# Kernel tuning notes

Hardware: AMD Instinct MI355X
Metric: run time of the kernel (lower is better)

## Reference

```python
import jax, jax.numpy as jnp
import numpy as np
from jax import lax

L, T, DM, DH = 4, 4096, 2048, 1024
MAX_PHASE = 6.28
EPS = 1e-5


def setup_inputs() -> dict:
    key = jax.random.key(0)
    ks = jax.random.split(key, 16)
    # LRU initializers (r_min=0, r_max=1)
    u1 = jax.random.uniform(ks[0], (L, DH))
    nu_log = jnp.log(-0.5 * jnp.log(u1))
    u2 = jax.random.uniform(ks[1], (L, DH))
    theta_log = jnp.log(MAX_PHASE * u2)
    abs_lam = jnp.exp(-jnp.exp(nu_log))  # |lambda|
    gamma_log = jnp.log(jnp.sqrt(1.0 - abs_lam ** 2))
    B_re = jax.random.normal(ks[2], (L, DH, DM)) / np.sqrt(2 * DM)
    B_im = jax.random.normal(ks[3], (L, DH, DM)) / np.sqrt(2 * DM)
    C_re = jax.random.normal(ks[4], (L, DM, DH)) / np.sqrt(DH)
    C_im = jax.random.normal(ks[5], (L, DM, DH)) / np.sqrt(DH)
    D = jax.random.normal(ks[6], (L, DM))
    bound = 1.0 / np.sqrt(DM)
    enc_w = jax.random.uniform(ks[7], (DM, DM), minval=-bound, maxval=bound)
    enc_b = jax.random.uniform(ks[8], (DM,), minval=-bound, maxval=bound)
    out1_w = jax.random.uniform(ks[9], (L, DM, DM), minval=-bound, maxval=bound)
    out1_b = jax.random.uniform(ks[10], (L, DM), minval=-bound, maxval=bound)
    out2_w = jax.random.uniform(ks[11], (L, DM, DM), minval=-bound, maxval=bound)
    out2_b = jax.random.uniform(ks[12], (L, DM), minval=-bound, maxval=bound)
    norm_w = jnp.ones((L, DM))
    norm_b = jnp.zeros((L, DM))
    x = jax.random.normal(ks[13], (T, DM))
    return dict(x=x, enc_w=enc_w, enc_b=enc_b, nu_log=nu_log, theta_log=theta_log,
                gamma_log=gamma_log, B_re=B_re, B_im=B_im, C_re=C_re, C_im=C_im,
                D=D, norm_w=norm_w, norm_b=norm_b, out1_w=out1_w, out1_b=out1_b,
                out2_w=out2_w, out2_b=out2_b)


def _lru(xn, nu, th, gl, br, bi, cr, ci, d):
    # xn: (T, DM) real -> (T, DM) real
    lam = jnp.exp(-jnp.exp(nu) + 1j * jnp.exp(th))          # (DH,) complex
    B_norm = (br + 1j * bi) * jnp.exp(gl)[:, None]           # (DH, DM)
    Bu = xn.astype(B_norm.dtype) @ B_norm.T                  # (T, DH) complex
    a = jnp.broadcast_to(lam, Bu.shape)
    def combine(e1, e2):
        a1, b1 = e1
        a2, b2 = e2
        return a1 * a2, a2 * b1 + b2
    _, h = lax.associative_scan(combine, (a, Bu), axis=0)    # h_t = lam*h_{t-1} + Bu_t
    C = cr + 1j * ci
    return (h @ C.T).real + xn * d


def _batchnorm(x, w, b):
    # training-mode BatchNorm1d over dim 0 (biased variance), matching torch
    mu = x.mean(axis=0)
    var = jnp.mean((x - mu) ** 2, axis=0)
    return (x - mu) / jnp.sqrt(var + EPS) * w + b


def _forward(x, enc_w, enc_b, nu_log, theta_log, gamma_log, B_re, B_im,
             C_re, C_im, D, norm_w, norm_b, out1_w, out1_b, out2_w, out2_b):
    x = x @ enc_w.T + enc_b
    def layer(carry, p):
        nu, th, gl, br, bi, cr, ci, d, nw, nb, w1, b1, w2, b2 = p
        xn = _batchnorm(carry, nw, nb)
        y = _lru(xn, nu, th, gl, br, bi, cr, ci, d)
        y = jax.nn.gelu(y, approximate=False)
        y = (y @ w1.T + b1) * jax.nn.sigmoid(y @ w2.T + b2)
        return carry + y, None
    x, _ = lax.scan(layer, x, (nu_log, theta_log, gamma_log, B_re, B_im,
                               C_re, C_im, D, norm_w, norm_b,
                               out1_w, out1_b, out2_w, out2_b))
    return x


def reference(x, enc_w, enc_b, nu_log, theta_log, gamma_log, B_re, B_im,
              C_re, C_im, D, norm_w, norm_b, out1_w, out1_b, out2_w, out2_b):
    return _forward(x, enc_w, enc_b, nu_log, theta_log, gamma_log, B_re, B_im,
                    C_re, C_im, D, norm_w, norm_b, out1_w, out1_b, out2_w, out2_b)
```

## Files before the change

### kernel.cpp

```cpp
#include <hip/hip_runtime.h>
#include <stdint.h>
#include <math.h>


#define LAYERS 4
#define TT     4096
#define DMODEL 2048
#define DHID   1024
#define NCHUNK 64
#define CLEN   64
#define KTILES 64

typedef unsigned short ushort_t;
typedef __attribute__((ext_vector_type(8))) _Float16 half8;
typedef __attribute__((ext_vector_type(4))) float    f32x4;

__device__ __forceinline__ unsigned pack2h(float a, float b) {
  _Float16 ha = (_Float16)a, hb = (_Float16)b;
  unsigned short ua = *(unsigned short*)&ha, ub = *(unsigned short*)&hb;
  return (unsigned)ua | ((unsigned)ub << 16);
}

__global__ __launch_bounds__(256)
void convert_h(const float* __restrict__ B0, const float* __restrict__ B1,
               int ldb, int NS, int KS, ushort_t* __restrict__ Hi)
{
  __shared__ float tile[128][33];
  const int mb  = blockIdx.x;
  const int kb  = blockIdx.y;
  const int tid = threadIdx.x;
  const int r0  = tid >> 3;
  const int c0  = (tid & 7) * 4;
#pragma unroll
  for (int rep = 0; rep < 4; ++rep) {
    const int rr = rep * 32 + r0;
    const int n  = mb * 128 + rr;
    const int k  = kb * 32 + c0;
    const float* bp; long idx;
    if (n >= NS)      { bp = B1; idx = (long)(n - NS) * ldb + k; }
    else if (k >= KS) { bp = B1; idx = (long)n * ldb + (k - KS); }
    else              { bp = B0; idx = (long)n * ldb + k; }
#pragma unroll
    for (int u = 0; u < 4; ++u) tile[rr][c0 + u] = bp[idx + u];
  }
  __syncthreads();
#pragma unroll
  for (int rep = 0; rep < 2; ++rep) {
    const int id2 = rep * 256 + tid;
    const int kg  = id2 >> 7;
    const int m   = id2 & 127;
    const long off = ((long)mb * KTILES + kb) * 4096 + (kg * 128 + m) * 8;
    unsigned hw[4];
#pragma unroll
    for (int p = 0; p < 4; ++p)
      hw[p] = pack2h(tile[m][kg * 8 + p * 2], tile[m][kg * 8 + p * 2 + 1]);
    *(uint4*)&Hi[off] = make_uint4(hw[0], hw[1], hw[2], hw[3]);
  }
}

__global__ __launch_bounds__(256)
void bn_convert(const float* __restrict__ carry, const float* __restrict__ stats,
                const float* __restrict__ nw, const float* __restrict__ nb,
                ushort_t* __restrict__ Hi)
{
  __shared__ float tile[128][33];
  const int mb  = blockIdx.x;
  const int kb  = blockIdx.y;
  const int tid = threadIdx.x;
  const int r0  = tid >> 3;
  const int c0  = (tid & 7) * 4;
  float mean[4], rstd[4], w_[4], b_[4];
#pragma unroll
  for (int u = 0; u < 4; ++u) {
    const int j = kb * 32 + c0 + u;
    const float mu = stats[j] * (1.0f / TT);
    const float va = fmaxf(stats[DMODEL + j] * (1.0f / TT) - mu * mu, 0.0f);
    mean[u] = mu; rstd[u] = rsqrtf(va + 1e-5f);
    w_[u] = nw[j]; b_[u] = nb[j];
  }
#pragma unroll
  for (int rep = 0; rep < 4; ++rep) {
    const int rr  = rep * 32 + r0;
    const long base = (long)(mb * 128 + rr) * 2048 + kb * 32 + c0;
#pragma unroll
    for (int u = 0; u < 4; ++u)
      tile[rr][c0 + u] = (carry[base + u] - mean[u]) * rstd[u] * w_[u] + b_[u];
  }
  __syncthreads();
#pragma unroll
  for (int rep = 0; rep < 2; ++rep) {
    const int id2 = rep * 256 + tid;
    const int kg  = id2 >> 7;
    const int m   = id2 & 127;
    const long off = ((long)mb * KTILES + kb) * 4096 + (kg * 128 + m) * 8;
    unsigned hw[4];
#pragma unroll
    for (int p = 0; p < 4; ++p)
      hw[p] = pack2h(tile[m][kg * 8 + p * 2], tile[m][kg * 8 + p * 2 + 1]);
    *(uint4*)&Hi[off] = make_uint4(hw[0], hw[1], hw[2], hw[3]);
  }
}

__global__ __launch_bounds__(256)
void scan3_convert(const float* __restrict__ loc,
                   const float* __restrict__ ccre, const float* __restrict__ ccim,
                   const float* __restrict__ nu_log, const float* __restrict__ th_log,
                   ushort_t* __restrict__ Hi)
{
  __shared__ float tile[128][33];
  const int mb  = blockIdx.x;
  const int kb  = blockIdx.y;
  const int tid = threadIdx.x;
  const int r0  = tid >> 3;
  const int c0  = (tid & 7) * 4;
  const int isim = (kb >= 32);
  const int c0l  = (mb * 2) & 1023;
  (void)c0l;
  float en[4], eth[4], cr0[4], ci0[4], cr1[4], ci1[4];
#pragma unroll
  for (int u = 0; u < 4; ++u) {
    const int col = kb * 32 + c0 + u;
    const int h   = col & 1023;
    en[u]  = expf(nu_log[h]);
    eth[u] = expf(th_log[h]);
    const int ch0 = mb * 2, ch1 = mb * 2 + 1;
    cr0[u] = ccre[ch0 * DHID + h]; ci0[u] = ccim[ch0 * DHID + h];
    cr1[u] = ccre[ch1 * DHID + h]; ci1[u] = ccim[ch1 * DHID + h];
  }
#pragma unroll
  for (int rep = 0; rep < 4; ++rep) {
    const int rr  = rep * 32 + r0;
    const int sel = rr >> 6;
    const float p = (float)((rr & 63) + 1);
    const long base = (long)(mb * 128 + rr) * 2048 + kb * 32 + c0;
#pragma unroll
    for (int u = 0; u < 4; ++u) {
      const float magp = expf(-p * en[u]);
      const float ang  = p * eth[u];
      float sv, cv;
      __sincosf(ang, &sv, &cv);
      const float pr = magp * cv, pi = magp * sv;
      const float cr_ = sel ? cr1[u] : cr0[u];
      const float ci_ = sel ? ci1[u] : ci0[u];
      const float L = loc[base + u];
      const float v = isim ? -(L + pr * ci_ + pi * cr_)
                           :  (L + pr * cr_ - pi * ci_);
      tile[rr][c0 + u] = v;
    }
  }
  __syncthreads();
#pragma unroll
  for (int rep = 0; rep < 2; ++rep) {
    const int id2 = rep * 256 + tid;
    const int kg  = id2 >> 7;
    const int m   = id2 & 127;
    const long off = ((long)mb * KTILES + kb) * 4096 + (kg * 128 + m) * 8;
    unsigned hw[4];
#pragma unroll
    for (int p2 = 0; p2 < 4; ++p2)
      hw[p2] = pack2h(tile[m][kg * 8 + p2 * 2], tile[m][kg * 8 + p2 * 2 + 1]);
    *(uint4*)&Hi[off] = make_uint4(hw[0], hw[1], hw[2], hw[3]);
  }
}

__global__ __launch_bounds__(256)
void e1_convert(const float* __restrict__ y, const ushort_t* __restrict__ xnT,
                const float* __restrict__ d, ushort_t* __restrict__ Hi)
{
  __shared__ float tile[128][33];
  const int mb  = blockIdx.x;
  const int kb  = blockIdx.y;
  const int tid = threadIdx.x;
  const int r0  = tid >> 3;
  const int c0  = (tid & 7) * 4;
#pragma unroll
  for (int rep = 0; rep < 4; ++rep) {
    const int rr  = rep * 32 + r0;
    const long base = (long)(mb * 128 + rr) * 2048 + kb * 32 + c0;
#pragma unroll
    for (int u = 0; u < 4; ++u) tile[rr][c0 + u] = y[base + u];
  }
  __syncthreads();
#pragma unroll
  for (int rep = 0; rep < 2; ++rep) {
    const int id2 = rep * 256 + tid;
    const int kg  = id2 >> 7;
    const int m   = id2 & 127;
    const long off = ((long)mb * KTILES + kb) * 4096 + (kg * 128 + m) * 8;
    const half8 xh = *(const half8*)&xnT[off];
    const float* dp = d + kb * 32 + kg * 8;
    unsigned hw[4];
#pragma unroll
    for (int p = 0; p < 4; ++p) {
      float g2[2];
#pragma unroll
      for (int e = 0; e < 2; ++e) {
        const int j = p * 2 + e;
        const float v = tile[m][kg * 8 + j] + (float)xh[j] * dp[j];
        g2[e] = 0.5f * v * (1.0f + erff(v * 0.70710678118654752440f));
      }
      hw[p] = pack2h(g2[0], g2[1]);
    }
    *(uint4*)&Hi[off] = make_uint4(hw[0], hw[1], hw[2], hw[3]);
  }
}

#define GLDS(gp, lp) __builtin_amdgcn_global_load_lds( \
    (__attribute__((address_space(1))) void*)(void*)(gp), \
    (__attribute__((address_space(3))) void*)(lp), 16, 0, 0)

__global__ __launch_bounds__(256)
void gemm_mfma(const ushort_t* __restrict__ Ahi, const ushort_t* __restrict__ Bhi,
               float* __restrict__ C, const float* __restrict__ bias,
               int epi, float* __restrict__ stats)
{
  __shared__ ushort_t S[2][16384];
  const int tid  = threadIdx.x;
  const int lane = tid & 63;
  const int wid  = tid >> 6;
  const int wm   = wid >> 1;
  const int wn   = wid & 1;

  const int bid = blockIdx.y * gridDim.x + blockIdx.x;
  const int xcd = bid & 7, idx = bid >> 3;
  const int mb  = ((xcd & 3) << 3) | (idx & 7);
  const int nb  = ((xcd >> 2) << 3) | (idx >> 3);

  f32x4 acc[4][4];
#pragma unroll
  for (int i = 0; i < 4; ++i)
#pragma unroll
    for (int j = 0; j < 4; ++j) acc[i][j] = (f32x4){0.f, 0.f, 0.f, 0.f};

  const ushort_t* ga = Ahi + (long)mb * KTILES * 4096 + tid * 8;
  const ushort_t* gb = Bhi + (long)nb * KTILES * 4096 + tid * 8;

  const int albase = ((lane >> 4) * 128 + wm * 64 + (lane & 15)) * 8;
  const int blbase = ((lane >> 4) * 128 + wn * 64 + (lane & 15)) * 8;

  half8 A0[4], B0[4], A1[4], B1[4];

#define STAGE(P) \
  GLDS(ga,        &S[P][tid * 8]); \
  GLDS(ga + 2048, &S[P][2048 + tid * 8]); \
  GLDS(ga + 4096, &S[P][4096 + tid * 8]); \
  GLDS(ga + 6144, &S[P][6144 + tid * 8]); \
  GLDS(gb,        &S[P][8192 + tid * 8]); \
  GLDS(gb + 2048, &S[P][10240 + tid * 8]); \
  GLDS(gb + 4096, &S[P][12288 + tid * 8]); \
  GLDS(gb + 6144, &S[P][14336 + tid * 8]); \
  ga += 8192; gb += 8192;

#define RD(P) \
  _Pragma("unroll") \
  for (int m = 0; m < 4; ++m) A0[m] = *(const half8*)&S[P][albase + m * 128]; \
  _Pragma("unroll") \
  for (int n = 0; n < 4; ++n) B0[n] = *(const half8*)&S[P][8192 + blbase + n * 128]; \
  _Pragma("unroll") \
  for (int m = 0; m < 4; ++m) A1[m] = *(const half8*)&S[P][4096 + albase + m * 128]; \
  _Pragma("unroll") \
  for (int n = 0; n < 4; ++n) B1[n] = *(const half8*)&S[P][12288 + blbase + n * 128];

#define MFMA16(A_, B_) \
  _Pragma("unroll") \
  for (int m = 0; m < 4; ++m) \
    _Pragma("unroll") \
    for (int n = 0; n < 4; ++n) \
      acc[m][n] = __builtin_amdgcn_mfma_f32_16x16x32_f16(A_[m], B_[n], acc[m][n], 0, 0, 0);

#define WAIT_VM_BAR(n) asm volatile("s_waitcnt vmcnt(" #n ")" ::: "memory"); \
  __builtin_amdgcn_sched_barrier(0); __builtin_amdgcn_s_barrier();
#define LGKM0_BAR asm volatile("s_waitcnt lgkmcnt(0)" ::: "memory"); \
  __builtin_amdgcn_sched_barrier(0); __builtin_amdgcn_s_barrier();

#define KSTEP(P) \
  WAIT_VM_BAR(8) \
  RD(P) \
  __builtin_amdgcn_s_setprio(1); \
  MFMA16(A0, B0) \
  MFMA16(A1, B1) \
  __builtin_amdgcn_s_setprio(0); \
  LGKM0_BAR \
  STAGE(P)

  STAGE(0)
  STAGE(1)
  for (int it = 0; it < 15; ++it) {
    KSTEP(0)
    KSTEP(1)
  }
  WAIT_VM_BAR(8)
  RD(0)
  __builtin_amdgcn_s_setprio(1);
  MFMA16(A0, B0)
  MFMA16(A1, B1)
  __builtin_amdgcn_s_setprio(0);
  WAIT_VM_BAR(0)
  RD(1)
  __builtin_amdgcn_s_setprio(1);
  MFMA16(A0, B0)
  MFMA16(A1, B1)
  __builtin_amdgcn_s_setprio(0);
#undef STAGE
#undef RD
#undef MFMA16
#undef WAIT_VM_BAR
#undef LGKM0_BAR
#undef KSTEP

  const int cn = lane & 15;
  const int cr = (lane >> 4) * 4;
  float s0[4] = {0.f, 0.f, 0.f, 0.f}, s1[4] = {0.f, 0.f, 0.f, 0.f};
#pragma unroll
  for (int m = 0; m < 4; ++m) {
    const long row = (long)mb * 128 + wm * 64 + m * 16 + cr;
#pragma unroll
    for (int n = 0; n < 4; ++n) {
      const int col = nb * 128 + wn * 64 + n * 16 + cn;
      const float bv = bias ? bias[col] : 0.0f;
      if (epi == 0) {
#pragma unroll
        for (int q = 0; q < 4; ++q) {
          const float v = acc[m][n][q] + bv;
          C[(row + q) * 2048 + col] = v;
          s0[n] += v; s1[n] += v * v;
        }
      } else {
#pragma unroll
        for (int q = 0; q < 4; ++q)
          C[(row + q) * 2048 + col] = acc[m][n][q] + bv;
      }
    }
  }
  if (stats) {
    __syncthreads();
    float* sred = (float*)&S[0][0];
    if (tid < 256) sred[tid] = 0.f;
    __syncthreads();
#pragma unroll
    for (int n = 0; n < 4; ++n) {
      const int lc = wn * 64 + n * 16 + cn;
      atomicAdd(&sred[lc], s0[n]);
      atomicAdd(&sred[128 + lc], s1[n]);
    }
    __syncthreads();
    if (tid < 128) {
      atomicAdd(&stats[nb * 128 + tid], sred[tid]);
      atomicAdd(&stats[DMODEL + nb * 128 + tid], sred[128 + tid]);
    }
  }
}

__global__ __launch_bounds__(256)
void gemm_dual(const ushort_t* __restrict__ Ahi, const ushort_t* __restrict__ B1t,
               const ushort_t* __restrict__ B2t,
               float* __restrict__ carry, const float* __restrict__ b1,
               const float* __restrict__ b2, float* __restrict__ stats)
{
  __shared__ ushort_t S[3][8192];
  const int tid  = threadIdx.x;
  const int lane = tid & 63;
  const int wid  = tid >> 6;
  const int wm   = wid >> 1;
  const int wn   = wid & 1;

  const int bid = blockIdx.y * gridDim.x + blockIdx.x;
  const int xcd = bid & 7, idx = bid >> 3;
  const int mb  = ((xcd & 3) << 3) | (idx & 7);
  const int nbb = ((xcd >> 2) << 4) | (idx >> 3);

  f32x4 acc1[4][2], acc2[4][2];
#pragma unroll
  for (int i = 0; i < 4; ++i)
#pragma unroll
    for (int j = 0; j < 2; ++j) {
      acc1[i][j] = (f32x4){0.f, 0.f, 0.f, 0.f};
      acc2[i][j] = (f32x4){0.f, 0.f, 0.f, 0.f};
    }

  const int nt = nbb >> 1;
  const int hb = nbb & 1;

  const ushort_t* ga = Ahi + (long)mb * KTILES * 4096 + tid * 8;
  const long boff = ((tid >> 6) * 128 + hb * 64 + (tid & 63)) * 8;
  const ushort_t* g1 = B1t + (long)nt * KTILES * 4096 + boff;
  const ushort_t* g2 = B2t + (long)nt * KTILES * 4096 + boff;

  const int albase = ((lane >> 4) * 128 + wm * 64 + (lane & 15)) * 8;
  const int blbase = ((lane >> 4) * 64 + wn * 32 + (lane & 15)) * 8;

  half8 Af[4], B1f[2], B2f[2];

#define STAGE(P) \
  GLDS(ga,        &S[P][tid * 8]); \
  GLDS(ga + 2048, &S[P][2048 + tid * 8]); \
  GLDS(g1,        &S[P][4096 + tid * 8]); \
  GLDS(g2,        &S[P][6144 + tid * 8]); \
  ga += 4096; g1 += 4096; g2 += 4096;

#define RD(P) \
  _Pragma("unroll") \
  for (int m = 0; m < 4; ++m) Af[m]  = *(const half8*)&S[P][albase + m * 128]; \
  _Pragma("unroll") \
  for (int n = 0; n < 2; ++n) B1f[n] = *(const half8*)&S[P][4096 + blbase + n * 128]; \
  _Pragma("unroll") \
  for (int n = 0; n < 2; ++n) B2f[n] = *(const half8*)&S[P][6144 + blbase + n * 128];

#define MFMA16D \
  __builtin_amdgcn_s_setprio(1); \
  _Pragma("unroll") \
  for (int m = 0; m < 4; ++m) \
    _Pragma("unroll") \
    for (int n = 0; n < 2; ++n) \
      acc1[m][n] = __builtin_amdgcn_mfma_f32_16x16x32_f16(Af[m], B1f[n], acc1[m][n], 0, 0, 0); \
  _Pragma("unroll") \
  for (int m = 0; m < 4; ++m) \
    _Pragma("unroll") \
    for (int n = 0; n < 2; ++n) \
      acc2[m][n] = __builtin_amdgcn_mfma_f32_16x16x32_f16(Af[m], B2f[n], acc2[m][n], 0, 0, 0); \
  __builtin_amdgcn_s_setprio(0);

#define WAITB(n) asm volatile("s_waitcnt vmcnt(" #n ") lgkmcnt(0)" ::: "memory"); \
  __builtin_amdgcn_sched_barrier(0); __builtin_amdgcn_s_barrier();

#define KSTEPD(PRD, PST) \
  WAITB(4) \
  STAGE(PST) \
  RD(PRD) \
  MFMA16D

  STAGE(0)
  STAGE(1)
  for (int it = 0; it < 20; ++it) {
    KSTEPD(0, 2)
    KSTEPD(1, 0)
    KSTEPD(2, 1)
  }
  KSTEPD(0, 2)
  KSTEPD(1, 0)
  WAITB(4)
  RD(2)
  MFMA16D
  WAITB(0)
  RD(0)
  MFMA16D
#undef STAGE
#undef RD
#undef MFMA16D
#undef WAITB
#undef KSTEPD

  const int cn = lane & 15;
  const int cr = (lane >> 4) * 4;
  float s0[2] = {0.f, 0.f}, s1[2] = {0.f, 0.f};
#pragma unroll
  for (int m = 0; m < 4; ++m) {
    const long row = (long)mb * 128 + wm * 64 + m * 16 + cr;
#pragma unroll
    for (int n = 0; n < 2; ++n) {
      const int col = nbb * 64 + wn * 32 + n * 16 + cn;
      const float b1v = b1[col], b2v = b2[col];
#pragma unroll
      for (int q = 0; q < 4; ++q) {
        const long idx2 = (row + q) * 2048 + col;
        const float t1v = acc1[m][n][q] + b1v;
        const float t2v = acc2[m][n][q] + b2v;
        const float v = carry[idx2] + t1v * (1.0f / (1.0f + expf(-t2v)));
        carry[idx2] = v;
        s0[n] += v; s1[n] += v * v;
      }
    }
  }
  if (stats) {
    __syncthreads();
    float* sred = (float*)&S[0][0];
    if (tid < 128) sred[tid] = 0.f;
    __syncthreads();
#pragma unroll
    for (int n = 0; n < 2; ++n) {
      const int lc = wn * 32 + n * 16 + cn;
      atomicAdd(&sred[lc], s0[n]);
      atomicAdd(&sred[64 + lc], s1[n]);
    }
    __syncthreads();
    if (tid < 64) {
      atomicAdd(&stats[nbb * 64 + tid], sred[tid]);
      atomicAdd(&stats[DMODEL + nbb * 64 + tid], sred[64 + tid]);
    }
  }
}

__device__ __forceinline__ void get_lam(const float* nu_log, const float* th_log,
                                        int h, float& lre, float& lim)
{
  const float mag = expf(-expf(nu_log[h]));
  const float th  = expf(th_log[h]);
  lre = mag * cosf(th);
  lim = mag * sinf(th);
}

__global__ void scan1(float* __restrict__ bu,
                      const float* __restrict__ nu_log, const float* __restrict__ th_log,
                      const float* __restrict__ gl_log)
{
  const int gid = blockIdx.x * 256 + threadIdx.x;
  const int c = gid >> 10, h = gid & 1023;
  float lre, lim; get_lam(nu_log, th_log, h, lre, lim);
  const float gamma = expf(gl_log[h]);
  float hr = 0.f, hi = 0.f;
  for (int i = 0; i < CLEN; ++i) {
    const long t = (long)c * CLEN + i;
    const float br_ = bu[t * 2048 + h] * gamma;
    const float bi_ = bu[t * 2048 + 1024 + h] * gamma;
    const float nr = lre * hr - lim * hi + br_;
    const float ni = lre * hi + lim * hr + bi_;
    hr = nr; hi = ni;
    bu[t * 2048 + h] = hr;
    bu[t * 2048 + 1024 + h] = hi;
  }
}

__global__ void scan2(const float* __restrict__ loc,
                      float* __restrict__ ccre, float* __restrict__ ccim,
                      const float* __restrict__ nu_log, const float* __restrict__ th_log)
{
  const int h = blockIdx.x * 256 + threadIdx.x;
  float lre, lim; get_lam(nu_log, th_log, h, lre, lim);
  float ar = lre, ai = lim;
  for (int s = 0; s < 6; ++s) { float nr = ar * ar - ai * ai, ni = 2.f * ar * ai; ar = nr; ai = ni; }
  float er = 0.f, ei = 0.f;
  for (int c = 0; c < NCHUNK; ++c) {
    ccre[c * DHID + h] = er; ccim[c * DHID + h] = ei;
    const long t = (long)c * CLEN + (CLEN - 1);
    const float nr = ar * er - ai * ei + loc[t * 2048 + h];
    const float ni = ar * ei + ai * er + loc[t * 2048 + 1024 + h];
    er = nr; ei = ni;
  }
}

__global__ void finalize(const float* __restrict__ carry, float* __restrict__ out)
{
  const long idx = (long)blockIdx.x * 256 + threadIdx.x;
  const float v = carry[idx];
  out[idx] = (v == v && fabsf(v) < 3.0e38f) ? v : 300000.0f;
}

__global__ void diagfill(float* __restrict__ out, float val)
{
  const long idx = (long)blockIdx.x * 256 + threadIdx.x;
  out[idx] = (idx == 0) ? val : 0.0f;
}

extern "C" void kernel_launch(void* const* d_in, const int* in_sizes, int n_in,
                              void* d_out, int out_size, void* d_ws, size_t ws_size,
                              hipStream_t stream)
{
  (void)out_size;
  const int EW = (TT * DMODEL) / 256;
  float* out = (float*)d_out;

  if (n_in != 17 || in_sizes[0] != TT * DMODEL) {
    diagfill<<<EW, 256, 0, stream>>>(out, (float)(1 << 18));
    return;
  }
  if (ws_size < 151600000ull) {
    diagfill<<<EW, 256, 0, stream>>>(out, (float)(1 << 12));
    return;
  }

  const float* x     = (const float*)d_in[0];
  const float* enc_w = (const float*)d_in[1];
  const float* enc_b = (const float*)d_in[2];
  const float* nu    = (const float*)d_in[3];
  const float* th    = (const float*)d_in[4];
  const float* gl    = (const float*)d_in[5];
  const float* Bre   = (const float*)d_in[6];
  const float* Bim   = (const float*)d_in[7];
  const float* Cre   = (const float*)d_in[8];
  const float* Cim   = (const float*)d_in[9];
  const float* Dd    = (const float*)d_in[10];
  const float* nw    = (const float*)d_in[11];
  const float* nb    = (const float*)d_in[12];
  const float* w1    = (const float*)d_in[13];
  const float* b1    = (const float*)d_in[14];
  const float* w2    = (const float*)d_in[15];
  const float* b2    = (const float*)d_in[16];

  char* ws = (char*)d_ws;
  float*    carry = (float*)(ws);
  ushort_t* AhiX  = (ushort_t*)(ws + 33554432);
  float*    buf1  = (float*)(ws + 67108864);
  ushort_t* Ahi   = (ushort_t*)(ws + 100663296);
  ushort_t* B2hi  = (ushort_t*)(ws + 117440512);
  ushort_t* Bhi   = (ushort_t*)(ws + 134217728);
  float*    ccre  = (float*)(ws + 150994944);
  float*    ccim  = (float*)(ws + 151257088);
  float*    stats = (float*)(ws + 151519232);

  const dim3 gcA(32, 64);
  const dim3 gcW(16, 64);
  const dim3 gg(32, 16);
  const dim3 gg2(32, 32);
  const int BIG = 1 << 30;

  hipMemsetAsync(stats, 0, 2 * DMODEL * sizeof(float), stream);
  convert_h<<<gcA, 256, 0, stream>>>(x, x, 2048, BIG, BIG, Ahi);
  convert_h<<<gcW, 256, 0, stream>>>(enc_w, enc_w, 2048, BIG, BIG, Bhi);
  gemm_mfma<<<gg, 256, 0, stream>>>(Ahi, Bhi, carry, enc_b, 0, stats);

  for (int l = 0; l < LAYERS; ++l) {
    const float* Brl = Bre + (size_t)l * DHID * DMODEL;
    const float* Bil = Bim + (size_t)l * DHID * DMODEL;
    const float* Crl = Cre + (size_t)l * DMODEL * DHID;
    const float* Cil = Cim + (size_t)l * DMODEL * DHID;
    const float* w1l = w1 + (size_t)l * DMODEL * DMODEL;
    const float* w2l = w2 + (size_t)l * DMODEL * DMODEL;

    bn_convert<<<gcA, 256, 0, stream>>>(carry, stats, nw + l * DMODEL,
                                        nb + l * DMODEL, AhiX);

    convert_h<<<gcW, 256, 0, stream>>>(Brl, Bil, 2048, 1024, BIG, Bhi);
    gemm_mfma<<<gg, 256, 0, stream>>>(AhiX, Bhi, buf1, nullptr, 3, nullptr);

    scan1<<<256, 256, 0, stream>>>(buf1, nu + l * DHID, th + l * DHID, gl + l * DHID);
    scan2<<<4, 256, 0, stream>>>(buf1, ccre, ccim, nu + l * DHID, th + l * DHID);

    convert_h<<<gcW, 256, 0, stream>>>(Crl, Cil, 1024, BIG, 1024, Bhi);
    scan3_convert<<<gcA, 256, 0, stream>>>(buf1, ccre, ccim, nu + l * DHID,
                                           th + l * DHID, Ahi);

    gemm_mfma<<<gg, 256, 0, stream>>>(Ahi, Bhi, buf1, nullptr, 3, nullptr);

    e1_convert<<<gcA, 256, 0, stream>>>(buf1, AhiX, Dd + l * DMODEL, Ahi);

    convert_h<<<gcW, 256, 0, stream>>>(w1l, w1l, 2048, BIG, BIG, Bhi);
    convert_h<<<gcW, 256, 0, stream>>>(w2l, w2l, 2048, BIG, BIG, B2hi);
    float* nstats = (l < LAYERS - 1) ? stats : nullptr;
    if (nstats) hipMemsetAsync(stats, 0, 2 * DMODEL * sizeof(float), stream);
    gemm_dual<<<gg2, 256, 0, stream>>>(Ahi, Bhi, B2hi, carry,
                                       b1 + l * DMODEL, b2 + l * DMODEL, nstats);
  }

  finalize<<<EW, 256, 0, stream>>>(carry, out);
}
```

Baseline: 1.307 ms.

## Fuse chunk-local LRU scan and GELU convert into GEMM epilogues with interleaved re/im layout

```diff
diff --git a/kernel.cpp b/kernel.cpp
--- a/kernel.cpp
+++ b/kernel.cpp
@@ -19,6 +19,15 @@
   _Float16 ha = (_Float16)a, hb = (_Float16)b;
   unsigned short ua = *(unsigned short*)&ha, ub = *(unsigned short*)&hb;
   return (unsigned)ua | ((unsigned)ub << 16);
+}
+
+__device__ __forceinline__ void get_lam(const float* nu_log, const float* th_log,
+                                        int h, float& lre, float& lim)
+{
+  const float mag = expf(-expf(nu_log[h]));
+  const float th  = expf(th_log[h]);
+  lre = mag * cosf(th);
+  lim = mag * sinf(th);
 }
 
 __global__ __launch_bounds__(256)
@@ -59,6 +68,75 @@
 }
 
 __global__ __launch_bounds__(256)
+void convert_ilv_rows(const float* __restrict__ P0, const float* __restrict__ P1,
+                      int ldb, ushort_t* __restrict__ Hi)
+{
+  __shared__ float tile[128][33];
+  const int mb  = blockIdx.x;
+  const int kb  = blockIdx.y;
+  const int tid = threadIdx.x;
+  const int r0  = tid >> 3;
+  const int c0  = (tid & 7) * 4;
+#pragma unroll
+  for (int rep = 0; rep < 4; ++rep) {
+    const int rr = rep * 32 + r0;
+    const int n  = mb * 128 + rr;
+    const float* bp = (n & 1) ? P1 : P0;
+    const long idx = (long)(n >> 1) * ldb + kb * 32 + c0;
+#pragma unroll
+    for (int u = 0; u < 4; ++u) tile[rr][c0 + u] = bp[idx + u];
+  }
+  __syncthreads();
+#pragma unroll
+  for (int rep = 0; rep < 2; ++rep) {
+    const int id2 = rep * 256 + tid;
+    const int kg  = id2 >> 7;
+    const int m   = id2 & 127;
+    const long off = ((long)mb * KTILES + kb) * 4096 + (kg * 128 + m) * 8;
+    unsigned hw[4];
+#pragma unroll
+    for (int p = 0; p < 4; ++p)
+      hw[p] = pack2h(tile[m][kg * 8 + p * 2], tile[m][kg * 8 + p * 2 + 1]);
+    *(uint4*)&Hi[off] = make_uint4(hw[0], hw[1], hw[2], hw[3]);
+  }
+}
+
+__global__ __launch_bounds__(256)
+void convert_ilv_cols(const float* __restrict__ P0, const float* __restrict__ P1,
+                      int ldb, ushort_t* __restrict__ Hi)
+{
+  __shared__ float tile[128][33];
+  const int mb  = blockIdx.x;
+  const int kb  = blockIdx.y;
+  const int tid = threadIdx.x;
+  const int r0  = tid >> 3;
+  const int c0  = (tid & 7) * 4;
+#pragma unroll
+  for (int rep = 0; rep < 4; ++rep) {
+    const int rr = rep * 32 + r0;
+    const int n  = mb * 128 + rr;
+    const long base = (long)n * ldb + ((kb * 32 + c0) >> 1);
+    tile[rr][c0 + 0] = P0[base];
+    tile[rr][c0 + 1] = P1[base];
+    tile[rr][c0 + 2] = P0[base + 1];
+    tile[rr][c0 + 3] = P1[base + 1];
+  }
+  __syncthreads();
+#pragma unroll
+  for (int rep = 0; rep < 2; ++rep) {
+    const int id2 = rep * 256 + tid;
+    const int kg  = id2 >> 7;
+    const int m   = id2 & 127;
+    const long off = ((long)mb * KTILES + kb) * 4096 + (kg * 128 + m) * 8;
+    unsigned hw[4];
+#pragma unroll
+    for (int p = 0; p < 4; ++p)
+      hw[p] = pack2h(tile[m][kg * 8 + p * 2], tile[m][kg * 8 + p * 2 + 1]);
+    *(uint4*)&Hi[off] = make_uint4(hw[0], hw[1], hw[2], hw[3]);
+  }
+}
+
+__global__ __launch_bounds__(256)
 void bn_convert(const float* __restrict__ carry, const float* __restrict__ stats,
                 const float* __restrict__ nw, const float* __restrict__ nb,
                 ushort_t* __restrict__ Hi)
@@ -113,19 +191,17 @@
   const int tid = threadIdx.x;
   const int r0  = tid >> 3;
   const int c0  = (tid & 7) * 4;
-  const int isim = (kb >= 32);
-  const int c0l  = (mb * 2) & 1023;
-  (void)c0l;
   float en[4], eth[4], cr0[4], ci0[4], cr1[4], ci1[4];
+  int   im[4];
 #pragma unroll
   for (int u = 0; u < 4; ++u) {
     const int col = kb * 32 + c0 + u;
-    const int h   = col & 1023;
+    const int h   = col >> 1;
+    im[u]  = col & 1;
     en[u]  = expf(nu_log[h]);
     eth[u] = expf(th_log[h]);
-    const int ch0 = mb * 2, ch1 = mb * 2 + 1;
-    cr0[u] = ccre[ch0 * DHID + h]; ci0[u] = ccim[ch0 * DHID + h];
-    cr1[u] = ccre[ch1 * DHID + h]; ci1[u] = ccim[ch1 * DHID + h];
+    cr0[u] = ccre[(mb * 2) * DHID + h];     ci0[u] = ccim[(mb * 2) * DHID + h];
+    cr1[u] = ccre[(mb * 2 + 1) * DHID + h]; ci1[u] = ccim[(mb * 2 + 1) * DHID + h];
   }
 #pragma unroll
   for (int rep = 0; rep < 4; ++rep) {
@@ -143,9 +219,8 @@
       const float cr_ = sel ? cr1[u] : cr0[u];
       const float ci_ = sel ? ci1[u] : ci0[u];
       const float L = loc[base + u];
-      const float v = isim ? -(L + pr * ci_ + pi * cr_)
-                           :  (L + pr * cr_ - pi * ci_);
-      tile[rr][c0 + u] = v;
+      tile[rr][c0 + u] = im[u] ? -(L + pr * ci_ + pi * cr_)
+                               :  (L + pr * cr_ - pi * ci_);
     }
   }
   __syncthreads();
@@ -163,48 +238,6 @@
   }
 }
 
-__global__ __launch_bounds__(256)
-void e1_convert(const float* __restrict__ y, const ushort_t* __restrict__ xnT,
-                const float* __restrict__ d, ushort_t* __restrict__ Hi)
-{
-  __shared__ float tile[128][33];
-  const int mb  = blockIdx.x;
-  const int kb  = blockIdx.y;
-  const int tid = threadIdx.x;
-  const int r0  = tid >> 3;
-  const int c0  = (tid & 7) * 4;
-#pragma unroll
-  for (int rep = 0; rep < 4; ++rep) {
-    const int rr  = rep * 32 + r0;
-    const long base = (long)(mb * 128 + rr) * 2048 + kb * 32 + c0;
-#pragma unroll
-    for (int u = 0; u < 4; ++u) tile[rr][c0 + u] = y[base + u];
-  }
-  __syncthreads();
-#pragma unroll
-  for (int rep = 0; rep < 2; ++rep) {
-    const int id2 = rep * 256 + tid;
-    const int kg  = id2 >> 7;
-    const int m   = id2 & 127;
-    const long off = ((long)mb * KTILES + kb) * 4096 + (kg * 128 + m) * 8;
-    const half8 xh = *(const half8*)&xnT[off];
-    const float* dp = d + kb * 32 + kg * 8;
-    unsigned hw[4];
-#pragma unroll
-    for (int p = 0; p < 4; ++p) {
-      float g2[2];
-#pragma unroll
-      for (int e = 0; e < 2; ++e) {
-        const int j = p * 2 + e;
-        const float v = tile[m][kg * 8 + j] + (float)xh[j] * dp[j];
-        g2[e] = 0.5f * v * (1.0f + erff(v * 0.70710678118654752440f));
-      }
-      hw[p] = pack2h(g2[0], g2[1]);
-    }
-    *(uint4*)&Hi[off] = make_uint4(hw[0], hw[1], hw[2], hw[3]);
-  }
-}
-
 #define GLDS(gp, lp) __builtin_amdgcn_global_load_lds( \
     (__attribute__((address_space(1))) void*)(void*)(gp), \
     (__attribute__((address_space(3))) void*)(lp), 16, 0, 0)
@@ -212,7 +245,11 @@
 __global__ __launch_bounds__(256)
 void gemm_mfma(const ushort_t* __restrict__ Ahi, const ushort_t* __restrict__ Bhi,
                float* __restrict__ C, const float* __restrict__ bias,
-               int epi, float* __restrict__ stats)
+               int epi, float* __restrict__ stats,
+               ushort_t* __restrict__ gT,
+               const float* __restrict__ dvec,
+               const float* __restrict__ nu_log, const float* __restrict__ th_log,
+               const float* __restrict__ gl_log)
 {
   __shared__ ushort_t S[2][16384];
   const int tid  = threadIdx.x;
@@ -310,43 +347,105 @@
 
   const int cn = lane & 15;
   const int cr = (lane >> 4) * 4;
-  float s0[4] = {0.f, 0.f, 0.f, 0.f}, s1[4] = {0.f, 0.f, 0.f, 0.f};
-#pragma unroll
-  for (int m = 0; m < 4; ++m) {
-    const long row = (long)mb * 128 + wm * 64 + m * 16 + cr;
-#pragma unroll
-    for (int n = 0; n < 4; ++n) {
-      const int col = nb * 128 + wn * 64 + n * 16 + cn;
-      const float bv = bias ? bias[col] : 0.0f;
-      if (epi == 0) {
+
+  if (epi == 0) {
+    float s0[4] = {0.f, 0.f, 0.f, 0.f}, s1[4] = {0.f, 0.f, 0.f, 0.f};
+#pragma unroll
+    for (int m = 0; m < 4; ++m) {
+      const long row = (long)mb * 128 + wm * 64 + m * 16 + cr;
+#pragma unroll
+      for (int n = 0; n < 4; ++n) {
+        const int col = nb * 128 + wn * 64 + n * 16 + cn;
+        const float bv = bias ? bias[col] : 0.0f;
 #pragma unroll
         for (int q = 0; q < 4; ++q) {
           const float v = acc[m][n][q] + bv;
           C[(row + q) * 2048 + col] = v;
           s0[n] += v; s1[n] += v * v;
         }
-      } else {
-#pragma unroll
-        for (int q = 0; q < 4; ++q)
-          C[(row + q) * 2048 + col] = acc[m][n][q] + bv;
       }
     }
-  }
-  if (stats) {
-    __syncthreads();
-    float* sred = (float*)&S[0][0];
-    if (tid < 256) sred[tid] = 0.f;
-    __syncthreads();
+    if (stats) {
+      __syncthreads();
+      float* sred = (float*)&S[0][0];
+      if (tid < 256) sred[tid] = 0.f;
+      __syncthreads();
+#pragma unroll
+      for (int n = 0; n < 4; ++n) {
+        const int lc = wn * 64 + n * 16 + cn;
+        atomicAdd(&sred[lc], s0[n]);
+        atomicAdd(&sred[128 + lc], s1[n]);
+      }
+      __syncthreads();
+      if (tid < 128) {
+        atomicAdd(&stats[nb * 128 + tid], sred[tid]);
+        atomicAdd(&stats[DMODEL + nb * 128 + tid], sred[128 + tid]);
+      }
+    }
+    return;
+  }
+
+  __syncthreads();
+  float* Lf = (float*)&S[0][0];
+#pragma unroll
+  for (int m = 0; m < 4; ++m) {
+    const int r = wm * 64 + m * 16 + cr;
 #pragma unroll
     for (int n = 0; n < 4; ++n) {
-      const int lc = wn * 64 + n * 16 + cn;
-      atomicAdd(&sred[lc], s0[n]);
-      atomicAdd(&sred[128 + lc], s1[n]);
-    }
-    __syncthreads();
+      const int c = wn * 64 + n * 16 + cn;
+#pragma unroll
+      for (int q = 0; q < 4; ++q)
+        Lf[(r + q) * 128 + c] = acc[m][n][q];
+    }
+  }
+  __syncthreads();
+
+  if (epi == 1) {
     if (tid < 128) {
-      atomicAdd(&stats[nb * 128 + tid], sred[tid]);
-      atomicAdd(&stats[DMODEL + nb * 128 + tid], sred[128 + tid]);
+      const int p  = tid & 63;
+      const int ch = tid >> 6;
+      const int hg = nb * 64 + p;
+      const float gamma = expf(gl_log[hg]);
+      float lre, lim; get_lam(nu_log, th_log, hg, lre, lim);
+      float hr = 0.f, hi = 0.f;
+      const long base = ((long)mb * 128 + ch * 64) * 2048 + nb * 128 + 2 * p;
+      for (int i = 0; i < 64; ++i) {
+        const float br_ = Lf[(ch * 64 + i) * 128 + 2 * p]     * gamma;
+        const float bi_ = Lf[(ch * 64 + i) * 128 + 2 * p + 1] * gamma;
+        const float nr = lre * hr - lim * hi + br_;
+        const float ni = lre * hi + lim * hr + bi_;
+        hr = nr; hi = ni;
+        *(float2*)&C[base + (long)i * 2048] = make_float2(hr, hi);
+      }
+    }
+    return;
+  }
+
+  {
+    const int cb = nb * 4;
+#pragma unroll
+    for (int c = 0; c < 8; ++c) {
+      const int chunk = c * 256 + tid;
+      const int m  = chunk & 127;
+      const int kg = (chunk >> 7) & 3;
+      const int lt = chunk >> 9;
+      const long off = ((long)mb * KTILES + cb + lt) * 4096 + (kg * 128 + m) * 8;
+      const half8 xh = *(const half8*)&gT[off];
+      const float* Lrow = &Lf[m * 128 + lt * 32 + kg * 8];
+      const float* dp = dvec + nb * 128 + lt * 32 + kg * 8;
+      unsigned hw[4];
+#pragma unroll
+      for (int p = 0; p < 4; ++p) {
+        float g2[2];
+#pragma unroll
+        for (int e = 0; e < 2; ++e) {
+          const int j = p * 2 + e;
+          const float v = Lrow[j] + (float)xh[j] * dp[j];
+          g2[e] = 0.5f * v * (1.0f + erff(v * 0.70710678118654752440f));
+        }
+        hw[p] = pack2h(g2[0], g2[1]);
+      }
+      *(uint4*)&gT[off] = make_uint4(hw[0], hw[1], hw[2], hw[3]);
     }
   }
 }
@@ -490,36 +589,6 @@
   }
 }
 
-__device__ __forceinline__ void get_lam(const float* nu_log, const float* th_log,
-                                        int h, float& lre, float& lim)
-{
-  const float mag = expf(-expf(nu_log[h]));
-  const float th  = expf(th_log[h]);
-  lre = mag * cosf(th);
-  lim = mag * sinf(th);
-}
-
-__global__ void scan1(float* __restrict__ bu,
-                      const float* __restrict__ nu_log, const float* __restrict__ th_log,
-                      const float* __restrict__ gl_log)
-{
-  const int gid = blockIdx.x * 256 + threadIdx.x;
-  const int c = gid >> 10, h = gid & 1023;
-  float lre, lim; get_lam(nu_log, th_log, h, lre, lim);
-  const float gamma = expf(gl_log[h]);
-  float hr = 0.f, hi = 0.f;
-  for (int i = 0; i < CLEN; ++i) {
-    const long t = (long)c * CLEN + i;
-    const float br_ = bu[t * 2048 + h] * gamma;
-    const float bi_ = bu[t * 2048 + 1024 + h] * gamma;
-    const float nr = lre * hr - lim * hi + br_;
-    const float ni = lre * hi + lim * hr + bi_;
-    hr = nr; hi = ni;
-    bu[t * 2048 + h] = hr;
-    bu[t * 2048 + 1024 + h] = hi;
-  }
-}
-
 __global__ void scan2(const float* __restrict__ loc,
                       float* __restrict__ ccre, float* __restrict__ ccim,
                       const float* __restrict__ nu_log, const float* __restrict__ th_log)
@@ -532,8 +601,8 @@
   for (int c = 0; c < NCHUNK; ++c) {
     ccre[c * DHID + h] = er; ccim[c * DHID + h] = ei;
     const long t = (long)c * CLEN + (CLEN - 1);
-    const float nr = ar * er - ai * ei + loc[t * 2048 + h];
-    const float ni = ar * ei + ai * er + loc[t * 2048 + 1024 + h];
+    const float nr = ar * er - ai * ei + loc[t * 2048 + 2 * h];
+    const float ni = ar * ei + ai * er + loc[t * 2048 + 2 * h + 1];
     er = nr; ei = ni;
   }
 }
@@ -606,7 +675,8 @@
   hipMemsetAsync(stats, 0, 2 * DMODEL * sizeof(float), stream);
   convert_h<<<gcA, 256, 0, stream>>>(x, x, 2048, BIG, BIG, Ahi);
   convert_h<<<gcW, 256, 0, stream>>>(enc_w, enc_w, 2048, BIG, BIG, Bhi);
-  gemm_mfma<<<gg, 256, 0, stream>>>(Ahi, Bhi, carry, enc_b, 0, stats);
+  gemm_mfma<<<gg, 256, 0, stream>>>(Ahi, Bhi, carry, enc_b, 0, stats,
+                                    nullptr, nullptr, nullptr, nullptr, nullptr);
 
   for (int l = 0; l < LAYERS; ++l) {
     const float* Brl = Bre + (size_t)l * DHID * DMODEL;
@@ -619,25 +689,26 @@
     bn_convert<<<gcA, 256, 0, stream>>>(carry, stats, nw + l * DMODEL,
                                         nb + l * DMODEL, AhiX);
 
-    convert_h<<<gcW, 256, 0, stream>>>(Brl, Bil, 2048, 1024, BIG, Bhi);
-    gemm_mfma<<<gg, 256, 0, stream>>>(AhiX, Bhi, buf1, nullptr, 3, nullptr);
-
-    scan1<<<256, 256, 0, stream>>>(buf1, nu + l * DHID, th + l * DHID, gl + l * DHID);
+    convert_ilv_rows<<<gcW, 256, 0, stream>>>(Brl, Bil, 2048, Bhi);
+    gemm_mfma<<<gg, 256, 0, stream>>>(AhiX, Bhi, buf1, nullptr, 1, nullptr,
+                                      nullptr, nullptr,
+                                      nu + l * DHID, th + l * DHID, gl + l * DHID);
+
     scan2<<<4, 256, 0, stream>>>(buf1, ccre, ccim, nu + l * DHID, th + l * DHID);
 
-    convert_h<<<gcW, 256, 0, stream>>>(Crl, Cil, 1024, BIG, 1024, Bhi);
+    convert_ilv_cols<<<gcW, 256, 0, stream>>>(Crl, Cil, 1024, Bhi);
     scan3_convert<<<gcA, 256, 0, stream>>>(buf1, ccre, ccim, nu + l * DHID,
                                            th + l * DHID, Ahi);
 
-    gemm_mfma<<<gg, 256, 0, stream>>>(Ahi, Bhi, buf1, nullptr, 3, nullptr);
-
-    e1_convert<<<gcA, 256, 0, stream>>>(buf1, AhiX, Dd + l * DMODEL, Ahi);
+    gemm_mfma<<<gg, 256, 0, stream>>>(Ahi, Bhi, nullptr, nullptr, 2, nullptr,
+                                      AhiX, Dd + l * DMODEL,
+                                      nullptr, nullptr, nullptr);
 
     convert_h<<<gcW, 256, 0, stream>>>(w1l, w1l, 2048, BIG, BIG, Bhi);
     convert_h<<<gcW, 256, 0, stream>>>(w2l, w2l, 2048, BIG, BIG, B2hi);
     float* nstats = (l < LAYERS - 1) ? stats : nullptr;
     if (nstats) hipMemsetAsync(stats, 0, 2 * DMODEL * sizeof(float), stream);
-    gemm_dual<<<gg2, 256, 0, stream>>>(Ahi, Bhi, B2hi, carry,
+    gemm_dual<<<gg2, 256, 0, stream>>>(AhiX, Bhi, B2hi, carry,
                                        b1 + l * DMODEL, b2 + l * DMODEL, nstats);
   }
 
```

Measured after the change: 1.231 ms. 5.8% less time.
